# Kernel optimization log

Measured on AMD Instinct MI355X. Metric: run time of the kernel, lower is better.

Reference implementation:

```python
import jax, jax.numpy as jnp
import numpy as np

EPS_RMS = 1e-4   # RunningMeanStd epsilon (mean=0, var=1 at init)
LN_EPS = 1e-5    # torch LayerNorm default
NUM_HEADS = 16


def _layernorm(x, g, b):
    m = x.mean(-1, keepdims=True)
    v = ((x - m) ** 2).mean(-1, keepdims=True)
    return (x - m) / jnp.sqrt(v + LN_EPS) * g + b


def _rms_normalize(a):
    # RunningMeanStd.normalize with mean=0, var=1: clip(a / sqrt(1+eps), -5, 5)
    return jnp.clip(a / jnp.sqrt(1.0 + EPS_RMS), -5.0, 5.0)


def _sinusoidal_pe(pos, d):
    # pos [...,] -> [..., d]; matches torch code: div_term over arange(d//2)
    div = jnp.exp(jnp.arange(d // 2, dtype=jnp.float32) * (-np.log(1000.0) / d))
    ang = pos[..., None] * div                         # [..., d//2]
    pe = jnp.zeros(pos.shape + (d,), dtype=jnp.float32)
    pe = pe.at[..., 0::2].set(jnp.sin(ang))
    pe = pe.at[..., 1::2].set(jnp.cos(ang))
    return pe


def _encoder_layer(xs, mask, Wqkv, bqkv, Wo, bo, g1, be1, g2, be2, Wf1, bf1, Wf2, bf2):
    # post-LN TransformerEncoderLayer with boolean attention mask [B,S,S]
    B, S, D = xs.shape
    hd = D // NUM_HEADS
    qkv = xs @ Wqkv.T + bqkv                           # [B,S,3D]
    q, k, v = jnp.split(qkv, 3, axis=-1)
    q = q.reshape(B, S, NUM_HEADS, hd).transpose(0, 2, 1, 3)
    k = k.reshape(B, S, NUM_HEADS, hd).transpose(0, 2, 1, 3)
    v = v.reshape(B, S, NUM_HEADS, hd).transpose(0, 2, 1, 3)
    scores = jnp.einsum('bhqd,bhkd->bhqk', q, k) / jnp.sqrt(jnp.float32(hd))
    scores = jnp.where(mask[:, None, :, :], -jnp.inf, scores)
    attn = jax.nn.softmax(scores, axis=-1)
    o = jnp.einsum('bhqk,bhkd->bhqd', attn, v).transpose(0, 2, 1, 3).reshape(B, S, D)
    o = o @ Wo.T + bo
    xs = _layernorm(xs + o, g1, be1)
    ff = jax.nn.gelu(xs @ Wf1.T + bf1, approximate=False) @ Wf2.T + bf2
    xs = _layernorm(xs + ff, g2, be2)
    return xs


def reference(x, w, y, W_nail, b_nail, W_cond, b_cond, Wqkv, bqkv, Wo, bo,
              ln1_g, ln1_b, ln2_g, ln2_b, W1, b1, W2, b2, W_ham, b_ham):
    B, Lx = x.shape[0], x.shape[1]
    n_w = w.shape[1] * w.shape[2]
    L = Lx + n_w + 1                                   # total_paragraph_length
    S = L - 1
    D = W_nail.shape[0]

    w_last = w[:, -1]                                  # [B, P, 6]

    # embed_x
    t = jnp.nan_to_num(x[..., 0])
    xc = jnp.nan_to_num(x)
    xx = _rms_normalize(xc)[..., 1:] @ W_nail.T + b_nail   # [B,Lx,D]
    xx = xx + _sinusoidal_pe(t, D)
    x_mask = jnp.isnan(x[..., 0])                      # [B,Lx]

    # embed_w
    wc = jnp.nan_to_num(w)
    wn = _rms_normalize(wc).reshape(B, -1, w.shape[-1])    # [B,Lw*P,6]
    ww = wn @ W_cond.T + b_cond                        # [B,Lw*P,D]

    tgt = jnp.concatenate([xx, ww], axis=1)            # [B,S,D]

    # custom per-batch boolean mask: causal, but columns [0,Lx) follow x padding mask
    causal = jnp.triu(jnp.ones((S, S), dtype=bool), 1)
    mask = jnp.broadcast_to(causal, (B, S, S))
    mask = mask.at[:, :, :Lx].set(x_mask[:, None, :])

    # global positional encoding added only on the w-token segment
    pe_g = _sinusoidal_pe(jnp.arange(L, dtype=jnp.float32), D)  # [L,D]
    tgt = tgt.at[:, Lx:].add(pe_g[Lx:L - 1])

    for i in range(Wqkv.shape[0]):
        tgt = _encoder_layer(tgt, mask, Wqkv[i], bqkv[i], Wo[i], bo[i],
                             ln1_g[i], ln1_b[i], ln2_g[i], ln2_b[i],
                             W1[i], b1[i], W2[i], b2[i])

    y_resid_hat = (tgt[:, -1] @ W_ham.T + b_ham).reshape(B, -1, 6)
    y_resid = jax.lax.stop_gradient(y - w_last)
    loss = jnp.mean((y_resid_hat - y_resid) ** 2)
    return loss


def setup_inputs() -> dict:
    key = jax.random.key(0)
    ks = jax.random.split(key, 16)
    NL, D, FF, HAM = 4, 1024, 4096, 144
    s = 0.02
    return {
        'x': jax.random.normal(ks[0], (8, 512, 64), jnp.float32),
        'w': jax.random.normal(ks[1], (8, 16, 24, 6), jnp.float32),
        'y': jax.random.normal(ks[2], (8, 24, 6), jnp.float32),
        'W_nail': jax.random.normal(ks[3], (D, 63), jnp.float32) * s,
        'b_nail': jnp.zeros((D,), jnp.float32),
        'W_cond': jax.random.normal(ks[4], (D, 6), jnp.float32) * s,
        'b_cond': jnp.zeros((D,), jnp.float32),
        'Wqkv': jax.random.normal(ks[5], (NL, 3 * D, D), jnp.float32) * s,
        'bqkv': jnp.zeros((NL, 3 * D), jnp.float32),
        'Wo': jax.random.normal(ks[6], (NL, D, D), jnp.float32) * s,
        'bo': jnp.zeros((NL, D), jnp.float32),
        'ln1_g': jnp.ones((NL, D), jnp.float32),
        'ln1_b': jnp.zeros((NL, D), jnp.float32),
        'ln2_g': jnp.ones((NL, D), jnp.float32),
        'ln2_b': jnp.zeros((NL, D), jnp.float32),
        'W1': jax.random.normal(ks[7], (NL, FF, D), jnp.float32) * s,
        'b1': jnp.zeros((NL, FF), jnp.float32),
        'W2': jax.random.normal(ks[8], (NL, D, FF), jnp.float32) * s,
        'b2': jnp.zeros((NL, D), jnp.float32),
        'W_ham': jax.random.normal(ks[9], (HAM, D), jnp.float32) * s,
        'b_ham': jnp.zeros((HAM,), jnp.float32),
    }
```

## Files before the change

kernel.cpp:

```cpp
#include <hip/hip_runtime.h>
#include <math.h>


#define B_      8
#define LX_     512
#define NW_     384
#define S_      896
#define D_      1024
#define H_      16
#define HD_     64
#define FF_     4096
#define HAM_    144

#define RMS_SCALE 0.9999500037496876f
#define PE_C     (-6.907755278982137f / 1024.0f)

typedef __bf16 bf16x4 __attribute__((ext_vector_type(4)));
typedef __bf16 bf16x8 __attribute__((ext_vector_type(8)));
typedef float  f32x4  __attribute__((ext_vector_type(4)));

static __device__ __forceinline__ float nan0(float v) { return (v != v) ? 0.0f : v; }

static __device__ __forceinline__ void async_copy16(const __bf16* g, __bf16* l) {
    __builtin_amdgcn_global_load_lds(
        (const __attribute__((address_space(1))) void*)g,
        (__attribute__((address_space(3))) void*)l, 16, 0, 0);
}

static __device__ __forceinline__ float fast_gelu(float x) {
    float x3 = x * x * x;
    float z = 0.7978845608028654f * x + 0.035677408136300125f * x3;
    float az = fabsf(z);
    float e = __expf(2.0f * az);
    float t = 1.0f - 2.0f / (e + 1.0f);
    t = (z < 0.0f) ? -t : t;
    return 0.5f * x * (1.0f + t);
}

__global__ __launch_bounds__(256) void convert4_kernel(
        const float* __restrict__ s0, const float* __restrict__ s1,
        const float* __restrict__ s2, const float* __restrict__ s3,
        __bf16* __restrict__ d0, __bf16* __restrict__ d1,
        __bf16* __restrict__ d2, __bf16* __restrict__ d3) {
    int blk = blockIdx.x;
    const float* src; __bf16* dst; int base;
    if (blk < 3072)      { src = s0; dst = d0; base = blk; }
    else if (blk < 4096) { src = s1; dst = d1; base = blk - 3072; }
    else if (blk < 8192) { src = s2; dst = d2; base = blk - 4096; }
    else                 { src = s3; dst = d3; base = blk - 8192; }
    int i = (base * 256 + threadIdx.x) * 4;
    float4 v = *(const float4*)&src[i];
    bf16x4 o = {(__bf16)v.x, (__bf16)v.y, (__bf16)v.z, (__bf16)v.w};
    *(bf16x4*)&dst[i] = o;
}

__global__ __launch_bounds__(256) void transpose_nail_kernel(
        const float* __restrict__ W_nail, float* __restrict__ WT) {
    int i = blockIdx.x * 256 + threadIdx.x;
    int d = i & 1023, kk = i >> 10;
    WT[kk * 1024 + d] = W_nail[d * 63 + kk];
}

__global__ __launch_bounds__(256) void embed_x_kernel(
        const float* __restrict__ x, const float* __restrict__ WT,
        const float* __restrict__ b_nail, __bf16* __restrict__ tgt_bf,
        int* __restrict__ xmask) {
    int row0 = blockIdx.x * 8;
    int tid = threadIdx.x;
    __shared__ float xn[8][64];
    __shared__ float ts[8];
#pragma unroll
    for (int it = 0; it < 2; ++it) {
        int i = tid + it * 256;
        int r = i >> 6, c = i & 63;
        float vv = x[(size_t)(row0 + r) * 64 + c];
        float v0 = nan0(vv);
        xn[r][c] = fminf(fmaxf(v0 * RMS_SCALE, -5.0f), 5.0f);
        if (c == 0) { ts[r] = v0; xmask[row0 + r] = (vv != vv) ? 1 : 0; }
    }
    __syncthreads();
    int d0 = tid * 4;
    float4 bz = *(const float4*)&b_nail[d0];
    float acc[8][4];
#pragma unroll
    for (int r = 0; r < 8; ++r) {
        acc[r][0] = bz.x; acc[r][1] = bz.y; acc[r][2] = bz.z; acc[r][3] = bz.w;
    }
    for (int k = 0; k < 63; ++k) {
        float4 wv = *(const float4*)&WT[k * 1024 + d0];
#pragma unroll
        for (int r = 0; r < 8; ++r) {
            float xv = xn[r][k + 1];
            acc[r][0] += xv * wv.x; acc[r][1] += xv * wv.y;
            acc[r][2] += xv * wv.z; acc[r][3] += xv * wv.w;
        }
    }
    float div[4];
#pragma unroll
    for (int j = 0; j < 4; ++j)
        div[j] = __expf((float)((d0 + j) >> 1) * PE_C);
#pragma unroll
    for (int r = 0; r < 8; ++r) {
        int row = row0 + r;
        int b = row >> 9, i = row & 511;
        float t = ts[r];
        bf16x4 ob;
#pragma unroll
        for (int j = 0; j < 4; ++j) {
            float ang = t * div[j];
            float pe = ((d0 + j) & 1) ? __cosf(ang) : __sinf(ang);
            ob[j] = (__bf16)(acc[r][j] + pe);
        }
        *(bf16x4*)&tgt_bf[((size_t)b * S_ + i) * D_ + d0] = ob;
    }
}

__global__ __launch_bounds__(256) void embed_w_kernel(
        const float* __restrict__ w, const float* __restrict__ W_cond,
        const float* __restrict__ b_cond, __bf16* __restrict__ tgt_bf) {
    int row = blockIdx.x;
    int b = row / NW_, j = row % NW_;
    const float* wr = w + (long)row * 6;
    float wn[6];
#pragma unroll
    for (int k = 0; k < 6; ++k)
        wn[k] = fminf(fmaxf(nan0(wr[k]) * RMS_SCALE, -5.0f), 5.0f);
    int tid = threadIdx.x;
    int d0 = tid * 4;
    float pos = (float)(LX_ + j);
    bf16x4 ob;
#pragma unroll
    for (int jj = 0; jj < 4; ++jj) {
        int d = d0 + jj;
        float acc = b_cond[d];
        const float* wc = W_cond + (long)d * 6;
#pragma unroll
        for (int k = 0; k < 6; ++k) acc += wn[k] * wc[k];
        float dv = expf((float)(d >> 1) * PE_C);
        float ang = pos * dv;
        ob[jj] = (__bf16)(acc + ((d & 1) ? cosf(ang) : sinf(ang)));
    }
    *(bf16x4*)&tgt_bf[((long)b * S_ + LX_ + j) * D_ + d0] = ob;
}

template <int MODE>
__global__ __launch_bounds__(256) void gemm_mfma(
        const __bf16* __restrict__ A, const __bf16* __restrict__ W,
        const float* __restrict__ bias,
        __bf16* __restrict__ Cb,
        __bf16* __restrict__ Cq, __bf16* __restrict__ Ck, __bf16* __restrict__ Cv,
        int M, int N, int K) {
    __shared__ __bf16 As[128 * 64];
    __shared__ __bf16 Bs[128 * 64];
    int tid = threadIdx.x;
    int wave = tid >> 6, lane = tid & 63;
    int m0 = blockIdx.y * 128, n0 = blockIdx.x * 128;
    int wm = (wave >> 1) * 64, wn = (wave & 1) * 64;

    int srow = wave * 32 + (lane >> 3);
    int scol = ((lane & 7) ^ (lane >> 3)) * 8;
    const __bf16* Ag = A + (size_t)(m0 + srow) * K + scol;
    const __bf16* Wg = W + (size_t)(n0 + srow) * K + scol;
    __bf16* Al = &As[wave * 2048];
    __bf16* Bl = &Bs[wave * 2048];

    f32x4 acc[4][4];
#pragma unroll
    for (int i = 0; i < 4; ++i)
#pragma unroll
        for (int j = 0; j < 4; ++j) acc[i][j] = 0.0f;

    int frow = lane & 15;
    int quad = lane >> 4;
    int sf = frow & 7;

    for (int k0 = 0; k0 < K; k0 += 64) {
        size_t off = (size_t)k0;
        async_copy16(Ag + off,                  Al);
        async_copy16(Ag + off + (size_t)8 * K,  Al + 512);
        async_copy16(Ag + off + (size_t)16 * K, Al + 1024);
        async_copy16(Ag + off + (size_t)24 * K, Al + 1536);
        async_copy16(Wg + off,                  Bl);
        async_copy16(Wg + off + (size_t)8 * K,  Bl + 512);
        async_copy16(Wg + off + (size_t)16 * K, Bl + 1024);
        async_copy16(Wg + off + (size_t)24 * K, Bl + 1536);
        __syncthreads();
#pragma unroll
        for (int ks = 0; ks < 2; ++ks) {
            int slot = ((quad + ks * 4) ^ sf) * 8;
            bf16x8 a[4], b[4];
#pragma unroll
            for (int mi = 0; mi < 4; ++mi)
                a[mi] = *(const bf16x8*)&As[(wm + mi * 16 + frow) * 64 + slot];
#pragma unroll
            for (int ni = 0; ni < 4; ++ni)
                b[ni] = *(const bf16x8*)&Bs[(wn + ni * 16 + frow) * 64 + slot];
#pragma unroll
            for (int mi = 0; mi < 4; ++mi)
#pragma unroll
                for (int ni = 0; ni < 4; ++ni)
                    acc[mi][ni] = __builtin_amdgcn_mfma_f32_16x16x32_bf16(
                        b[ni], a[mi], acc[mi][ni], 0, 0, 0);
        }
        __syncthreads();
    }

    int mrow_l = lane & 15;
    int nq = (lane >> 4) * 4;
#pragma unroll
    for (int ni = 0; ni < 4; ++ni) {
        int cg0 = n0 + wn + ni * 16 + nq;
        float4 bv = *(const float4*)&bias[cg0];
        float bz[4] = {bv.x, bv.y, bv.z, bv.w};
#pragma unroll
        for (int mi = 0; mi < 4; ++mi) {
            int rg = m0 + wm + mi * 16 + mrow_l;
            float vv[4];
#pragma unroll
            for (int r = 0; r < 4; ++r) {
                float v = acc[mi][ni][r] + bz[r];
                if (MODE == 1) v = fast_gelu(v);
                vv[r] = v;
            }
            bf16x4 o = {(__bf16)vv[0], (__bf16)vv[1], (__bf16)vv[2], (__bf16)vv[3]};
            if (MODE == 2) {
                int which = cg0 >> 10;
                int h = (cg0 & 1023) >> 6;
                int e = cg0 & 63;
                int bb = rg / S_, s = rg % S_;
                __bf16* dst = (which == 0) ? Cq : (which == 1) ? Ck : Cv;
                *(bf16x4*)&dst[(((size_t)bb * H_ + h) * S_ + s) * HD_ + e] = o;
            } else {
                *(bf16x4*)&Cb[(size_t)rg * N + cg0] = o;
            }
        }
    }
}

__global__ __launch_bounds__(256) void attn_mfma(
        const __bf16* __restrict__ q, const __bf16* __restrict__ k,
        const __bf16* __restrict__ v, const int* __restrict__ xmask,
        __bf16* __restrict__ ctx) {
    __shared__ __bf16 Ks[64][72];
    __shared__ __bf16 Vt[64][66];
    __shared__ __bf16 Ps[4][16][72];
    __shared__ float mb[LX_];
    int tid = threadIdx.x;
    int wave = tid >> 6, lane = tid & 63;
    int frow = lane & 15, quad = lane >> 4;
    int blk = blockIdx.x;
    int qt = blk % 14;
    int bh = blk / 14;
    int b = bh >> 4, h = bh & 15;
    int q0 = qt * 64;
    int q0w = q0 + wave * 16;
    size_t base = (size_t)bh * S_ * HD_;

    for (int i = tid; i < LX_; i += 256)
        mb[i] = xmask[(b << 9) + i] ? -INFINITY : 0.0f;

    const __bf16* qrow = q + base + (size_t)(q0w + frow) * HD_ + quad * 8;
    bf16x8 aq0 = *(const bf16x8*)qrow;
    bf16x8 aq1 = *(const bf16x8*)(qrow + 32);

    f32x4 o[4];
#pragma unroll
    for (int dt = 0; dt < 4; ++dt) o[dt] = 0.0f;
    float mrow[4] = {-INFINITY, -INFINITY, -INFINITY, -INFINITY};
    float lrow[4] = {0.0f, 0.0f, 0.0f, 0.0f};

    int kend = (q0 >= LX_) ? (q0 + 64) : LX_;

    int sr = tid >> 2;
    int sc = (tid & 3) * 8;
    const __bf16* kg = k + base + (size_t)sr * HD_ + sc;
    const __bf16* vg = v + base + (size_t)sr * HD_ + sc;

    for (int k0 = 0; k0 < kend; k0 += 64) {
        {
            size_t off = (size_t)k0 * HD_;
            bf16x8 k0v = *(const bf16x8*)(kg + off);
            bf16x8 k1v = *(const bf16x8*)(kg + off + 32);
            *(bf16x8*)&Ks[sr][sc] = k0v;
            *(bf16x8*)&Ks[sr][sc + 32] = k1v;
            bf16x8 v0v = *(const bf16x8*)(vg + off);
            bf16x8 v1v = *(const bf16x8*)(vg + off + 32);
#pragma unroll
            for (int j = 0; j < 8; ++j) {
                Vt[sc + j][sr] = v0v[j];
                Vt[sc + 32 + j][sr] = v1v[j];
            }
        }
        __syncthreads();

        f32x4 scr[4];
#pragma unroll
        for (int nt = 0; nt < 4; ++nt) {
            bf16x8 bk0 = *(const bf16x8*)&Ks[nt * 16 + frow][quad * 8];
            bf16x8 bk1 = *(const bf16x8*)&Ks[nt * 16 + frow][32 + quad * 8];
            f32x4 z = 0.0f;
            z = __builtin_amdgcn_mfma_f32_16x16x32_bf16(aq0, bk0, z, 0, 0, 0);
            z = __builtin_amdgcn_mfma_f32_16x16x32_bf16(aq1, bk1, z, 0, 0, 0);
            scr[nt] = z;
        }

        float tmax[4] = {-INFINITY, -INFINITY, -INFINITY, -INFINITY};
#pragma unroll
        for (int nt = 0; nt < 4; ++nt) {
            int kj = k0 + nt * 16 + frow;
            float bias = (kj < LX_) ? mb[kj] : 0.0f;
#pragma unroll
            for (int r = 0; r < 4; ++r) {
                float s = scr[nt][r] * 0.125f + bias;
                if (kj >= LX_ && kj > q0w + quad * 4 + r) s = -INFINITY;
                scr[nt][r] = s;
                tmax[r] = fmaxf(tmax[r], s);
            }
        }
#pragma unroll
        for (int off = 1; off < 16; off <<= 1)
#pragma unroll
            for (int r = 0; r < 4; ++r)
                tmax[r] = fmaxf(tmax[r], __shfl_xor(tmax[r], off, 64));

        float alpha[4], rsum[4];
#pragma unroll
        for (int r = 0; r < 4; ++r) {
            float nm = fmaxf(mrow[r], tmax[r]);
            alpha[r] = (nm == -INFINITY) ? 1.0f : __expf(mrow[r] - nm);
            mrow[r] = nm;
            rsum[r] = 0.0f;
        }
#pragma unroll
        for (int nt = 0; nt < 4; ++nt) {
#pragma unroll
            for (int r = 0; r < 4; ++r) {
                float s = scr[nt][r];
                float p = (s == -INFINITY) ? 0.0f : __expf(s - mrow[r]);
                rsum[r] += p;
                Ps[wave][quad * 4 + r][nt * 16 + frow] = (__bf16)p;
            }
        }
#pragma unroll
        for (int off = 1; off < 16; off <<= 1)
#pragma unroll
            for (int r = 0; r < 4; ++r)
                rsum[r] += __shfl_xor(rsum[r], off, 64);
#pragma unroll
        for (int r = 0; r < 4; ++r)
            lrow[r] = lrow[r] * alpha[r] + rsum[r];
#pragma unroll
        for (int dt = 0; dt < 4; ++dt)
#pragma unroll
            for (int r = 0; r < 4; ++r)
                o[dt][r] *= alpha[r];

        bf16x8 ap0 = *(const bf16x8*)&Ps[wave][frow][quad * 8];
        bf16x8 ap1 = *(const bf16x8*)&Ps[wave][frow][32 + quad * 8];
#pragma unroll
        for (int dt = 0; dt < 4; ++dt) {
            bf16x8 bv0 = *(const bf16x8*)&Vt[dt * 16 + frow][quad * 8];
            bf16x8 bv1 = *(const bf16x8*)&Vt[dt * 16 + frow][32 + quad * 8];
            o[dt] = __builtin_amdgcn_mfma_f32_16x16x32_bf16(ap0, bv0, o[dt], 0, 0, 0);
            o[dt] = __builtin_amdgcn_mfma_f32_16x16x32_bf16(ap1, bv1, o[dt], 0, 0, 0);
        }
        __syncthreads();
    }

#pragma unroll
    for (int r = 0; r < 4; ++r) {
        float inv = (lrow[r] > 0.0f) ? 1.0f / lrow[r] : 0.0f;
        int qg = q0w + quad * 4 + r;
        size_t ob = ((size_t)b * S_ + qg) * D_ + h * HD_;
#pragma unroll
        for (int dt = 0; dt < 4; ++dt)
            ctx[ob + dt * 16 + frow] = (__bf16)(o[dt][r] * inv);
    }
}

__global__ __launch_bounds__(256) void add_ln_kernel(
        __bf16* __restrict__ xs_bf, const __bf16* __restrict__ o,
        const float* __restrict__ g, const float* __restrict__ bb) {
    long row = blockIdx.x;
    __bf16* xr = xs_bf + row * D_;
    const __bf16* orr = o + row * D_;
    int tid = threadIdx.x;
    bf16x4 a4 = *(const bf16x4*)&xr[tid * 4];
    bf16x4 b4v = *(const bf16x4*)&orr[tid * 4];
    float vv[4];
#pragma unroll
    for (int j = 0; j < 4; ++j) vv[j] = (float)a4[j] + (float)b4v[j];
    float s = vv[0] + vv[1] + vv[2] + vv[3];
    __shared__ float red[4];
    __shared__ float stat;
#pragma unroll
    for (int off = 32; off; off >>= 1) s += __shfl_down(s, off, 64);
    if ((tid & 63) == 0) red[tid >> 6] = s;
    __syncthreads();
    if (tid == 0) stat = (red[0] + red[1] + red[2] + red[3]) * (1.0f / 1024.0f);
    __syncthreads();
    float mean = stat;
    float d[4];
    float s2 = 0.0f;
#pragma unroll
    for (int j = 0; j < 4; ++j) { d[j] = vv[j] - mean; s2 += d[j] * d[j]; }
    __syncthreads();
#pragma unroll
    for (int off = 32; off; off >>= 1) s2 += __shfl_down(s2, off, 64);
    if ((tid & 63) == 0) red[tid >> 6] = s2;
    __syncthreads();
    if (tid == 0) stat = (red[0] + red[1] + red[2] + red[3]) * (1.0f / 1024.0f);
    __syncthreads();
    float inv = 1.0f / sqrtf(stat + 1e-5f);
    float4 gg = *(const float4*)&g[tid * 4];
    float4 bv = *(const float4*)&bb[tid * 4];
    float g4[4] = {gg.x, gg.y, gg.z, gg.w};
    float b4[4] = {bv.x, bv.y, bv.z, bv.w};
    bf16x4 ob;
#pragma unroll
    for (int j = 0; j < 4; ++j) ob[j] = (__bf16)(d[j] * inv * g4[j] + b4[j]);
    *(bf16x4*)&xr[tid * 4] = ob;
}

__global__ __launch_bounds__(256) void head_kernel(
        const __bf16* __restrict__ tgt_bf, const float* __restrict__ W_ham,
        const float* __restrict__ b_ham, float* __restrict__ out) {
    int b = blockIdx.x;
    int tid = threadIdx.x;
    __shared__ float xr[D_];
    const __bf16* row = tgt_bf + ((long)b * S_ + (S_ - 1)) * D_;
    for (int i = tid; i < D_; i += 256) xr[i] = (float)row[i];
    __syncthreads();
    for (int n = tid; n < HAM_; n += 256) {
        float acc = b_ham[n];
        const float* wr = W_ham + (long)n * D_;
        for (int kk = 0; kk < D_; ++kk) acc += xr[kk] * wr[kk];
        out[b * HAM_ + n] = acc;
    }
}

__global__ __launch_bounds__(256) void loss_kernel(
        const float* __restrict__ head_out, const float* __restrict__ y,
        const float* __restrict__ w, float* __restrict__ out) {
    int tid = threadIdx.x;
    float acc = 0.0f;
    for (int i = tid; i < B_ * HAM_; i += 256) {
        int b = i / HAM_, r = i % HAM_;
        float w_last = w[((long)b * 16 + 15) * HAM_ + r];
        float resid = y[i] - w_last;
        float dd = head_out[i] - resid;
        acc += dd * dd;
    }
    __shared__ float red[4];
#pragma unroll
    for (int off = 32; off; off >>= 1) acc += __shfl_down(acc, off, 64);
    if ((tid & 63) == 0) red[tid >> 6] = acc;
    __syncthreads();
    if (tid == 0)
        out[0] = (red[0] + red[1] + red[2] + red[3]) * (1.0f / (B_ * HAM_));
}

extern "C" void kernel_launch(void* const* d_in, const int* in_sizes, int n_in,
                              void* d_out, int out_size, void* d_ws, size_t ws_size,
                              hipStream_t stream) {
    const float* x      = (const float*)d_in[0];
    const float* w      = (const float*)d_in[1];
    const float* y      = (const float*)d_in[2];
    const float* W_nail = (const float*)d_in[3];
    const float* b_nail = (const float*)d_in[4];
    const float* W_cond = (const float*)d_in[5];
    const float* b_cond = (const float*)d_in[6];
    const float* Wqkv   = (const float*)d_in[7];
    const float* bqkv   = (const float*)d_in[8];
    const float* Wo     = (const float*)d_in[9];
    const float* bo     = (const float*)d_in[10];
    const float* ln1_g  = (const float*)d_in[11];
    const float* ln1_b  = (const float*)d_in[12];
    const float* ln2_g  = (const float*)d_in[13];
    const float* ln2_b  = (const float*)d_in[14];
    const float* W1     = (const float*)d_in[15];
    const float* b1     = (const float*)d_in[16];
    const float* W2     = (const float*)d_in[17];
    const float* b2     = (const float*)d_in[18];
    const float* W_ham  = (const float*)d_in[19];
    const float* b_ham  = (const float*)d_in[20];

    float* ws = (float*)d_ws;
    const long SEG = (long)B_ * S_ * D_;
    float*  W_nailT = ws;
    __bf16* tmp_bf = (__bf16*)(ws + SEG);
    __bf16* tgt_bf = (__bf16*)(ws + 2 * SEG);
    __bf16* ctx_bf = (__bf16*)(ws + 2 * SEG + SEG / 2);
    __bf16* qb     = (__bf16*)(ws + 3 * SEG);
    __bf16* kb     = (__bf16*)(ws + 3 * SEG + SEG / 2);
    __bf16* vb     = (__bf16*)(ws + 4 * SEG);
    __bf16* ffh_bf = (__bf16*)(ws + 2 * SEG + SEG / 2);
    __bf16* wbf    = (__bf16*)(ws + 4 * SEG + SEG / 2);
    int*    xmask    = (int*)(ws + 4 * SEG + SEG / 2 + 6291456);
    float*  head_out = ws + 4 * SEG + SEG / 2 + 6291456 + 4096;

    __bf16* wqkv_bf = wbf;
    __bf16* wo_bf   = wbf + 3145728;
    __bf16* w1_bf   = wbf + 4194304;
    __bf16* w2_bf   = wbf + 8388608;

    const int M = B_ * S_;

    transpose_nail_kernel<<<252, 256, 0, stream>>>(W_nail, W_nailT);
    embed_x_kernel<<<B_ * LX_ / 8, 256, 0, stream>>>(x, W_nailT, b_nail, tgt_bf, xmask);
    embed_w_kernel<<<B_ * NW_, 256, 0, stream>>>(w, W_cond, b_cond, tgt_bf);

    for (int L = 0; L < 4; ++L) {
        const int NQ = 3 * D_ * D_, NO = D_ * D_, N1 = FF_ * D_, N2 = D_ * FF_;
        convert4_kernel<<<12288, 256, 0, stream>>>(
            Wqkv + (size_t)L * NQ, Wo + (size_t)L * NO,
            W1 + (size_t)L * N1, W2 + (size_t)L * N2,
            wqkv_bf, wo_bf, w1_bf, w2_bf);

        gemm_mfma<2><<<dim3(3 * D_ / 128, M / 128), 256, 0, stream>>>(
            tgt_bf, wqkv_bf, bqkv + (size_t)L * 3 * D_,
            nullptr, qb, kb, vb, M, 3 * D_, D_);
        attn_mfma<<<B_ * H_ * (S_ / 64), 256, 0, stream>>>(qb, kb, vb, xmask, ctx_bf);
        gemm_mfma<0><<<dim3(D_ / 128, M / 128), 256, 0, stream>>>(
            ctx_bf, wo_bf, bo + (size_t)L * D_,
            tmp_bf, nullptr, nullptr, nullptr, M, D_, D_);
        add_ln_kernel<<<M, 256, 0, stream>>>(tgt_bf, tmp_bf,
            ln1_g + (size_t)L * D_, ln1_b + (size_t)L * D_);
        gemm_mfma<1><<<dim3(FF_ / 128, M / 128), 256, 0, stream>>>(
            tgt_bf, w1_bf, b1 + (size_t)L * FF_,
            ffh_bf, nullptr, nullptr, nullptr, M, FF_, D_);
        gemm_mfma<0><<<dim3(D_ / 128, M / 128), 256, 0, stream>>>(
            ffh_bf, w2_bf, b2 + (size_t)L * D_,
            tmp_bf, nullptr, nullptr, nullptr, M, D_, FF_);
        add_ln_kernel<<<M, 256, 0, stream>>>(tgt_bf, tmp_bf,
            ln2_g + (size_t)L * D_, ln2_b + (size_t)L * D_);
    }

    head_kernel<<<B_, 256, 0, stream>>>(tgt_bf, W_ham, b_ham, head_out);
    loss_kernel<<<1, 256, 0, stream>>>(head_out, y, w, (float*)d_out);
}
```

Measured before the change: 1.798 ms.

## Replace GEMM with 256-row, 8-wave, double-buffered phased MFMA pipeline

Replaces the single-buffered 128x128 GEMM with a 512-thread kernel using 256xBN tiles, double-buffered LDS, and a four-phase schedule. Async global-to-LDS loads for tile t+2 are interleaved with MFMA work on the current tile, using explicit vmcnt waits, barriers and setprio. The goal is to hide load latency and raise arithmetic intensity per block. In exchange it uses more LDS and registers per block, and M=7168 gives fewer blocks, which may hurt occupancy and tail balance.

```diff
diff --git a/kernel.cpp b/kernel.cpp
--- a/kernel.cpp
+++ b/kernel.cpp
@@ -143,78 +143,168 @@
     *(bf16x4*)&tgt_bf[((long)b * S_ + LX_ + j) * D_ + d0] = ob;
 }
 
-template <int MODE>
-__global__ __launch_bounds__(256) void gemm_mfma(
+
+#define LDA(BUF, MH) do {                                                      \
+    _Pragma("unroll")                                                          \
+    for (int i_ = 0; i_ < 4; ++i_) {                                           \
+        const int row_ = (MH) * 128 + wr * 64 + i_ * 16 + frow;                \
+        _Pragma("unroll")                                                      \
+        for (int k_ = 0; k_ < 2; ++k_)                                         \
+            a[i_][k_] = *(const bf16x8*)&As[BUF][row_ * 64 +                   \
+                (((quad + k_ * 4) ^ sf) * 8)];                                 \
+    }                                                                          \
+} while (0)
+
+#define LDB(BUF, NH) do {                                                      \
+    _Pragma("unroll")                                                          \
+    for (int j_ = 0; j_ < NJ; ++j_) {                                          \
+        const int row_ = (BN == 256)                                           \
+            ? ((NH) * 128 + j_ * 16 + wc * 32 + frow)                          \
+            : ((NH) * 64 + wc * 16 + frow);                                    \
+        _Pragma("unroll")                                                      \
+        for (int k_ = 0; k_ < 2; ++k_)                                         \
+            b[(NH) * NJ + j_][k_] = *(const bf16x8*)&Bs[BUF][row_ * 64 +       \
+                (((quad + k_ * 4) ^ sf) * 8)];                                 \
+    }                                                                          \
+} while (0)
+
+#define MMA(MH, NH) do {                                                       \
+    _Pragma("unroll")                                                          \
+    for (int i_ = 0; i_ < 4; ++i_)                                             \
+        _Pragma("unroll")                                                      \
+        for (int j_ = 0; j_ < NJ; ++j_)                                        \
+            _Pragma("unroll")                                                  \
+            for (int k_ = 0; k_ < 2; ++k_)                                     \
+                acc[(MH) * 4 + i_][(NH) * NJ + j_] =                           \
+                    __builtin_amdgcn_mfma_f32_16x16x32_bf16(                   \
+                        b[(NH) * NJ + j_][k_], a[i_][k_],                      \
+                        acc[(MH) * 4 + i_][(NH) * NJ + j_], 0, 0, 0);          \
+} while (0)
+
+#define STAGE_A(BUF, H, KT) do {                                               \
+    const __bf16* g_ = Ag + (size_t)((H) * 128) * K + ((size_t)(KT) << 6);     \
+    async_copy16(g_, &As[BUF][((H) * 128) * 64 + dst8]);                       \
+    async_copy16(g_ + ((size_t)K << 6), &As[BUF][((H) * 128 + 64) * 64 + dst8]); \
+} while (0)
+
+#define STAGE_B(BUF, H, KT) do {                                               \
+    if constexpr (BN == 256) {                                                 \
+        const __bf16* g_ = Wg + (size_t)((H) * 128) * K + ((size_t)(KT) << 6); \
+        async_copy16(g_, &Bs[BUF][((H) * 128) * 64 + dst8]);                   \
+        async_copy16(g_ + ((size_t)K << 6),                                    \
+                     &Bs[BUF][((H) * 128 + 64) * 64 + dst8]);                  \
+    } else {                                                                   \
+        const __bf16* g_ = Wg + (size_t)((H) * 64) * K + ((size_t)(KT) << 6);  \
+        async_copy16(g_, &Bs[BUF][((H) * 64) * 64 + dst8]);                    \
+    }                                                                          \
+} while (0)
+
+#define PHASE_SYNC() do {                                                      \
+    __builtin_amdgcn_sched_barrier(0);                                         \
+    __builtin_amdgcn_s_barrier();                                              \
+    asm volatile("s_waitcnt lgkmcnt(0)" ::: "memory");                         \
+    __builtin_amdgcn_sched_barrier(0);                                         \
+} while (0)
+
+#define PHASE_END() do {                                                       \
+    __builtin_amdgcn_sched_barrier(0);                                         \
+    __builtin_amdgcn_s_barrier();                                              \
+} while (0)
+
+#define VM_MAIN do {                                                           \
+    if constexpr (BN == 256) { asm volatile("s_waitcnt vmcnt(6)" ::: "memory"); } \
+    else                     { asm volatile("s_waitcnt vmcnt(4)" ::: "memory"); } \
+} while (0)
+#define VM_ZERO asm volatile("s_waitcnt vmcnt(0)" ::: "memory")
+#define VM_NONE ((void)0)
+
+#define GTILE(S1, S2, VMOP) do {                                               \
+    const int bf_ = t & 1;                                                     \
+                          \
+    LDA(bf_, 0); LDB(bf_, 0);                                                  \
+    if (S1) STAGE_A(bf_ ^ 1, 1, t + 1);                                        \
+    PHASE_SYNC();                                                              \
+    __builtin_amdgcn_s_setprio(1); MMA(0, 0); __builtin_amdgcn_s_setprio(0);   \
+    PHASE_END();                                                               \
+                    \
+    LDB(bf_, 1);                                                               \
+    if (S2) STAGE_B(bf_, 0, t + 2);                                            \
+    PHASE_SYNC();                                                              \
+    __builtin_amdgcn_s_setprio(1); MMA(0, 1); __builtin_amdgcn_s_setprio(0);   \
+    PHASE_END();                                                               \
+                                     \
+    LDA(bf_, 1);                                                               \
+    if (S2) STAGE_A(bf_, 0, t + 2);                                            \
+    PHASE_SYNC();                                                              \
+    __builtin_amdgcn_s_setprio(1); MMA(1, 0); __builtin_amdgcn_s_setprio(0);   \
+    PHASE_END();                                                               \
+            \
+    if (S2) STAGE_B(bf_, 1, t + 2);                                            \
+    VMOP;                                                                      \
+    PHASE_SYNC();                                                              \
+    __builtin_amdgcn_s_setprio(1); MMA(1, 1); __builtin_amdgcn_s_setprio(0);   \
+    PHASE_END();                                                               \
+} while (0)
+
+template <int BN, int MODE>
+__global__ __launch_bounds__(512, 2) void gemm8p(
         const __bf16* __restrict__ A, const __bf16* __restrict__ W,
         const float* __restrict__ bias,
         __bf16* __restrict__ Cb,
         __bf16* __restrict__ Cq, __bf16* __restrict__ Ck, __bf16* __restrict__ Cv,
         int M, int N, int K) {
-    __shared__ __bf16 As[128 * 64];
-    __shared__ __bf16 Bs[128 * 64];
-    int tid = threadIdx.x;
-    int wave = tid >> 6, lane = tid & 63;
-    int m0 = blockIdx.y * 128, n0 = blockIdx.x * 128;
-    int wm = (wave >> 1) * 64, wn = (wave & 1) * 64;
-
-    int srow = wave * 32 + (lane >> 3);
-    int scol = ((lane & 7) ^ (lane >> 3)) * 8;
-    const __bf16* Ag = A + (size_t)(m0 + srow) * K + scol;
-    const __bf16* Wg = W + (size_t)(n0 + srow) * K + scol;
-    __bf16* Al = &As[wave * 2048];
-    __bf16* Bl = &Bs[wave * 2048];
-
-    f32x4 acc[4][4];
-#pragma unroll
-    for (int i = 0; i < 4; ++i)
-#pragma unroll
-        for (int j = 0; j < 4; ++j) acc[i][j] = 0.0f;
-
-    int frow = lane & 15;
-    int quad = lane >> 4;
-    int sf = frow & 7;
-
-    for (int k0 = 0; k0 < K; k0 += 64) {
-        size_t off = (size_t)k0;
-        async_copy16(Ag + off,                  Al);
-        async_copy16(Ag + off + (size_t)8 * K,  Al + 512);
-        async_copy16(Ag + off + (size_t)16 * K, Al + 1024);
-        async_copy16(Ag + off + (size_t)24 * K, Al + 1536);
-        async_copy16(Wg + off,                  Bl);
-        async_copy16(Wg + off + (size_t)8 * K,  Bl + 512);
-        async_copy16(Wg + off + (size_t)16 * K, Bl + 1024);
-        async_copy16(Wg + off + (size_t)24 * K, Bl + 1536);
-        __syncthreads();
-#pragma unroll
-        for (int ks = 0; ks < 2; ++ks) {
-            int slot = ((quad + ks * 4) ^ sf) * 8;
-            bf16x8 a[4], b[4];
-#pragma unroll
-            for (int mi = 0; mi < 4; ++mi)
-                a[mi] = *(const bf16x8*)&As[(wm + mi * 16 + frow) * 64 + slot];
-#pragma unroll
-            for (int ni = 0; ni < 4; ++ni)
-                b[ni] = *(const bf16x8*)&Bs[(wn + ni * 16 + frow) * 64 + slot];
-#pragma unroll
-            for (int mi = 0; mi < 4; ++mi)
-#pragma unroll
-                for (int ni = 0; ni < 4; ++ni)
-                    acc[mi][ni] = __builtin_amdgcn_mfma_f32_16x16x32_bf16(
-                        b[ni], a[mi], acc[mi][ni], 0, 0, 0);
-        }
-        __syncthreads();
-    }
-
-    int mrow_l = lane & 15;
-    int nq = (lane >> 4) * 4;
-#pragma unroll
-    for (int ni = 0; ni < 4; ++ni) {
-        int cg0 = n0 + wn + ni * 16 + nq;
+    constexpr int NI = BN / 64;
+    constexpr int NJ = NI / 2;
+    static_assert(BN == 256 || BN == 128, "BN");
+    __shared__ __attribute__((aligned(16))) __bf16 As[2][256 * 64];
+    __shared__ __attribute__((aligned(16))) __bf16 Bs[2][BN * 64];
+
+    const int tid = threadIdx.x;
+    const int wave = tid >> 6, lane = tid & 63;
+    const int wr = wave >> 2, wc = wave & 3;
+    const int frow = lane & 15, quad = lane >> 4;
+    const int sf = frow & 7;
+    const int m0 = blockIdx.y * 256, n0 = blockIdx.x * BN;
+
+    const int sr = tid >> 3;
+    const int scol = ((tid & 7) ^ (sr & 7)) * 8;
+    const __bf16* Ag = A + (size_t)(m0 + sr) * K + scol;
+    const __bf16* Wg = W + (size_t)(n0 + sr) * K + scol;
+    const int dst8 = tid * 8;
+
+    f32x4 acc[8][NI];
+#pragma unroll
+    for (int i = 0; i < 8; ++i)
+#pragma unroll
+        for (int j = 0; j < NI; ++j) acc[i][j] = 0.0f;
+    bf16x8 a[4][2];
+    bf16x8 b[NI][2];
+
+    const int NT = K >> 6;
+
+    STAGE_B(0, 0, 0); STAGE_A(0, 0, 0); STAGE_B(0, 1, 0); STAGE_A(0, 1, 0);
+    STAGE_B(1, 0, 1); STAGE_A(1, 0, 1); STAGE_B(1, 1, 1);
+    VM_MAIN;
+    __builtin_amdgcn_s_barrier();
+
+    int t = 0;
+    for (; t < NT - 2; ++t) { GTILE(1, 1, VM_MAIN); }
+    GTILE(1, 0, VM_ZERO);
+    ++t;
+    GTILE(0, 0, VM_NONE);
+
+#pragma unroll
+    for (int ni = 0; ni < NI; ++ni) {
+        int cg0;
+        if constexpr (BN == 256)
+            cg0 = n0 + (ni >> 1) * 128 + (ni & 1) * 16 + wc * 32 + quad * 4;
+        else
+            cg0 = n0 + ni * 64 + wc * 16 + quad * 4;
         float4 bv = *(const float4*)&bias[cg0];
         float bz[4] = {bv.x, bv.y, bv.z, bv.w};
 #pragma unroll
-        for (int mi = 0; mi < 4; ++mi) {
-            int rg = m0 + wm + mi * 16 + mrow_l;
+        for (int mi = 0; mi < 8; ++mi) {
+            int rg = m0 + (mi >> 2) * 128 + wr * 64 + (mi & 3) * 16 + frow;
             float vv[4];
 #pragma unroll
             for (int r = 0; r < 4; ++r) {
@@ -228,8 +318,8 @@
                 int h = (cg0 & 1023) >> 6;
                 int e = cg0 & 63;
                 int bb = rg / S_, s = rg % S_;
-                __bf16* dst = (which == 0) ? Cq : (which == 1) ? Ck : Cv;
-                *(bf16x4*)&dst[(((size_t)bb * H_ + h) * S_ + s) * HD_ + e] = o;
+                __bf16* dstp = (which == 0) ? Cq : (which == 1) ? Ck : Cv;
+                *(bf16x4*)&dstp[(((size_t)bb * H_ + h) * S_ + s) * HD_ + e] = o;
             } else {
                 *(bf16x4*)&Cb[(size_t)rg * N + cg0] = o;
             }
@@ -517,19 +607,19 @@
             W1 + (size_t)L * N1, W2 + (size_t)L * N2,
             wqkv_bf, wo_bf, w1_bf, w2_bf);
 
-        gemm_mfma<2><<<dim3(3 * D_ / 128, M / 128), 256, 0, stream>>>(
+        gemm8p<256, 2><<<dim3(3 * D_ / 256, M / 256), 512, 0, stream>>>(
             tgt_bf, wqkv_bf, bqkv + (size_t)L * 3 * D_,
             nullptr, qb, kb, vb, M, 3 * D_, D_);
         attn_mfma<<<B_ * H_ * (S_ / 64), 256, 0, stream>>>(qb, kb, vb, xmask, ctx_bf);
-        gemm_mfma<0><<<dim3(D_ / 128, M / 128), 256, 0, stream>>>(
+        gemm8p<128, 0><<<dim3(D_ / 128, M / 256), 512, 0, stream>>>(
             ctx_bf, wo_bf, bo + (size_t)L * D_,
             tmp_bf, nullptr, nullptr, nullptr, M, D_, D_);
         add_ln_kernel<<<M, 256, 0, stream>>>(tgt_bf, tmp_bf,
             ln1_g + (size_t)L * D_, ln1_b + (size_t)L * D_);
-        gemm_mfma<1><<<dim3(FF_ / 128, M / 128), 256, 0, stream>>>(
+        gemm8p<256, 1><<<dim3(FF_ / 256, M / 256), 512, 0, stream>>>(
             tgt_bf, w1_bf, b1 + (size_t)L * FF_,
             ffh_bf, nullptr, nullptr, nullptr, M, FF_, D_);
-        gemm_mfma<0><<<dim3(D_ / 128, M / 128), 256, 0, stream>>>(
+        gemm8p<128, 0><<<dim3(D_ / 128, M / 256), 512, 0, stream>>>(
             ffh_bf, w2_bf, b2 + (size_t)L * D_,
             tmp_bf, nullptr, nullptr, nullptr, M, D_, FF_);
         add_ln_kernel<<<M, 256, 0, stream>>>(tgt_bf, tmp_bf,
```

After: 1.874 ms. +4.2%, slower.
